# Kernel optimization log

Hardware: AMD Instinct MI355X
Metric: run time of the kernel (lower is better)

The kernel has to match this reference:

```python
import jax, jax.numpy as jnp
import numpy as np

B, N, C, H = 64, 197, 768, 12
CH = C // H            # 64 head dim
RC = CH // 2           # 32 reduced channel
RN = N // 8            # 24 reduced tokens
TOPK_COEF = 8
BUDGET = int(np.ceil(0.25 * N))   # 50
BASIS_THRESH = 0.02
MP_SCALE = H ** -0.5               # MaskPredictor: num_heads**-0.5 (as in source)
ATTN_SCALE = CH ** -0.5
LN_EPS = 1e-5


def _ln(x, g, b):
    mu = x.mean(-1, keepdims=True)
    var = ((x - mu) ** 2).mean(-1, keepdims=True)
    return (x - mu) * jax.lax.rsqrt(var + LN_EPS) * g + b


def _keep_topk(x, k):
    # zero all but the k largest along last axis (tie-break by value threshold)
    kth = jax.lax.top_k(x, k)[0][..., -1:]
    return jnp.where(x >= kth, x, 0.0)


def setup_inputs() -> dict:
    key = jax.random.key(0)
    ks = jax.random.split(key, 20)
    d = {}
    d['x'] = jax.random.normal(ks[0], (B, N, C), jnp.float32)
    s = 0.02
    d['Wqkv'] = jax.random.normal(ks[1], (C, 3 * C), jnp.float32) * s
    d['Wcq'] = jax.random.normal(ks[2], (CH, RC), jnp.float32) * s
    d['bcq'] = jnp.zeros((RC,), jnp.float32)
    d['Wck'] = jax.random.normal(ks[3], (CH, RC), jnp.float32) * s
    d['bck'] = jnp.zeros((RC,), jnp.float32)
    d['proj_n'] = jax.random.normal(ks[4], (N, RN), jnp.float32) * s
    d['proj_back_n'] = jax.random.normal(ks[5], (N, RN), jnp.float32) * s
    d['Wproj'] = jax.random.normal(ks[6], (C, C), jnp.float32) * s
    d['bproj'] = jnp.zeros((C,), jnp.float32)
    d['g1'] = jnp.ones((C,), jnp.float32)
    d['b1'] = jnp.zeros((C,), jnp.float32)
    d['g2'] = jnp.ones((C,), jnp.float32)
    d['b2'] = jnp.zeros((C,), jnp.float32)
    d['W1'] = jax.random.normal(ks[7], (C, 4 * C), jnp.float32) * s
    d['bfc1'] = jnp.zeros((4 * C,), jnp.float32)
    d['W2'] = jax.random.normal(ks[8], (4 * C, C), jnp.float32) * s
    d['bfc2'] = jnp.zeros((C,), jnp.float32)
    return d


def reference(x, Wqkv, Wcq, bcq, Wck, bck, proj_n, proj_back_n, Wproj, bproj,
              g1, b1, g2, b2, W1, bfc1, W2, bfc2):
    h = _ln(x, g1, b1)
    qkv = (h @ Wqkv).reshape(B, N, 3, H, CH).transpose(2, 0, 3, 1, 4)  # [3,B,H,N,CH]
    q, k, v = qkv[0], qkv[1], qkv[2]

    # ---- MaskPredictor (eval path) ----
    qp = q @ Wcq + bcq                                # [B,H,N,RC]
    kp = k @ Wck + bck                                # [B,H,N,RC]
    kk = jnp.einsum('bhnc,nr->bhcr', kp, proj_n)      # [B,H,RC,RN]
    cheap = jnp.einsum('bhnc,bhcr->bhnr', qp, kk) * MP_SCALE
    cheap = cheap[:, :, 1:, :]                        # drop cls query row
    basis_coef = jax.nn.softmax(cheap, axis=-1)       # [B,H,N-1,RN]
    basis_coef = _keep_topk(basis_coef, TOPK_COEF)
    basis = jnp.abs(proj_back_n.T)                    # [RN,N]
    basis = jnp.where(basis > BASIS_THRESH, basis, 0.0)
    approx_attn = basis_coef @ basis                  # [B,H,N-1,N]
    kth = jax.lax.top_k(approx_attn, BUDGET)[0][..., -1:]
    mask = approx_attn >= kth                         # [B,H,N-1,N] bool
    cls_mask = jnp.ones((B, H, 1, N), bool)
    attn_mask = jnp.concatenate([cls_mask, mask], axis=2)  # [B,H,N,N]

    # ---- masked full attention ----
    attn = jnp.einsum('bhqc,bhkc->bhqk', q * ATTN_SCALE, k)
    attn = jnp.where(attn_mask, attn, -jnp.inf)
    attn = jax.nn.softmax(attn, axis=-1)
    out = jnp.einsum('bhqk,bhkc->bhqc', attn, v)
    out = out.transpose(0, 2, 1, 3).reshape(B, N, C)
    out = out @ Wproj + bproj

    x = x + out                                       # skip_lam = 1.0
    h2 = _ln(x, g2, b2)
    mlp = jax.nn.gelu(h2 @ W1 + bfc1, approximate=False) @ W2 + bfc2
    x = x + mlp
    return x
```

## Files before the change

### kernel.cpp

```cpp
#include <hip/hip_runtime.h>
#include <math.h>
#include <float.h>

#define B_ 64
#define N_ 197
#define C_ 768
#define H_ 12
#define CH_ 64
#define RC_ 32
#define RN_ 24

typedef __attribute__((ext_vector_type(8))) short short8;
typedef __attribute__((ext_vector_type(4))) float f32x4;
typedef __attribute__((address_space(3))) void  lds_void;
typedef __attribute__((address_space(1))) const void g_void;

__device__ __forceinline__ float warp_sum(float v){
  #pragma unroll
  for(int o=32;o>=1;o>>=1) v += __shfl_xor(v,o);
  return v;
}
__device__ __forceinline__ float warp_max(float v){
  #pragma unroll
  for(int o=32;o>=1;o>>=1) v = fmaxf(v,__shfl_xor(v,o));
  return v;
}
__device__ __forceinline__ unsigned short f2bf(float f){
  union{float f; unsigned u;} c; c.f = f;
  unsigned r = c.u + 0x7FFF + ((c.u>>16)&1);
  return (unsigned short)(r>>16);
}
__device__ __forceinline__ float bf2f(unsigned short u){
  union{unsigned u; float f;} c; c.u = ((unsigned)u)<<16; return c.f;
}

__global__ __launch_bounds__(256) void ln_kernel(const float* __restrict__ x,
    const float* __restrict__ g, const float* __restrict__ bb, unsigned short* __restrict__ out){
  int r = blockIdx.x; int tid = threadIdx.x;
  const float* xr = x + (size_t)r*C_;
  float v0=xr[tid], v1=xr[tid+256], v2=xr[tid+512];
  __shared__ float red[8];
  float s = warp_sum(v0+v1+v2);
  if((tid&63)==0) red[tid>>6]=s;
  __syncthreads();
  float mu = (red[0]+red[1]+red[2]+red[3]) * (1.f/768.f);
  float d0=v0-mu,d1=v1-mu,d2=v2-mu;
  float s2 = warp_sum(d0*d0+d1*d1+d2*d2);
  if((tid&63)==0) red[4+(tid>>6)]=s2;
  __syncthreads();
  float rinv = rsqrtf((red[4]+red[5]+red[6]+red[7])*(1.f/768.f)+1e-5f);
  unsigned short* orow = out + (size_t)r*C_;
  orow[tid]     = f2bf(d0*rinv*g[tid]    +bb[tid]);
  orow[tid+256] = f2bf(d1*rinv*g[tid+256]+bb[tid+256]);
  orow[tid+512] = f2bf(d2*rinv*g[tid+512]+bb[tid+512]);
}

__global__ __launch_bounds__(256) void wtrans_kernel(const float* __restrict__ in,
    unsigned short* __restrict__ out, int K, int N){
  __shared__ float tile[32][33];
  int n0 = blockIdx.x*32, k0 = blockIdx.y*32;
  int tx = threadIdx.x&31, ty = threadIdx.x>>5;
  #pragma unroll
  for(int i=0;i<4;++i) tile[ty+8*i][tx] = in[(size_t)(k0+ty+8*i)*N + n0+tx];
  __syncthreads();
  #pragma unroll
  for(int i=0;i<4;++i) out[(size_t)(n0+ty+8*i)*K + k0+tx] = f2bf(tile[tx][ty+8*i]);
}

__global__ __launch_bounds__(256) void wcprep_kernel(const float* __restrict__ Wcq,
    const float* __restrict__ Wck, unsigned short* __restrict__ WcqT,
    unsigned short* __restrict__ WckT){
  int t = blockIdx.x*256 + threadIdx.x;
  if(t < 2048){
    int c = t>>6, k = t&63;
    WcqT[t] = f2bf(Wcq[k*32+c]);
    WckT[t] = f2bf(Wck[k*32+c]);
  }
}

template<int ACT, int RESID, int OUTBF16>
__global__ __launch_bounds__(256) void gemm_bf16(
    const unsigned short* __restrict__ A, const unsigned short* __restrict__ WT,
    const float* __restrict__ bias, const float* __restrict__ resid,
    void* __restrict__ Cout, int M, int K, int Nc){
  __shared__ unsigned short As[2*128*32];
  __shared__ unsigned short Bs[2*128*32];
  int tid = threadIdx.x, lane = tid&63, wid = tid>>6;
  int m0 = blockIdx.y*128, n0 = blockIdx.x*128;
  int wr = wid>>1, wc = wid&1;
  int lm = lane&15, lg = lane>>4;
  int row0 = tid>>2,         kc0 = (tid&3)*8;
  int row1 = (256+tid)>>2,   kc1 = (tid&3)*8;
  int ar0 = m0+row0; if(ar0 > M-1) ar0 = M-1;
  int ar1 = m0+row1; if(ar1 > M-1) ar1 = M-1;
  const unsigned short* gA0 = A  + (size_t)ar0*K + kc0;
  const unsigned short* gA1 = A  + (size_t)ar1*K + kc1;
  const unsigned short* gB0 = WT + (size_t)(n0+row0)*K + kc0;
  const unsigned short* gB1 = WT + (size_t)(n0+row1)*K + kc1;
  unsigned short* lA0 = As + (wid*64)*8;
  unsigned short* lA1 = As + (256 + wid*64)*8;
  unsigned short* lB0 = Bs + (wid*64)*8;
  unsigned short* lB1 = Bs + (256 + wid*64)*8;

#define STAGE_(buf, kt) do{ \
    __builtin_amdgcn_global_load_lds((g_void*)(gA0 + (kt)), (lds_void*)(lA0 + (buf)*4096), 16, 0, 0); \
    __builtin_amdgcn_global_load_lds((g_void*)(gB0 + (kt)), (lds_void*)(lB0 + (buf)*4096), 16, 0, 0); \
    __builtin_amdgcn_global_load_lds((g_void*)(gA1 + (kt)), (lds_void*)(lA1 + (buf)*4096), 16, 0, 0); \
    __builtin_amdgcn_global_load_lds((g_void*)(gB1 + (kt)), (lds_void*)(lB1 + (buf)*4096), 16, 0, 0); \
  }while(0)

  f32x4 acc[4][4] = {};
  const int nt = K/32;
  STAGE_(0, 0);
  __syncthreads();
  for(int t=0; t<nt; t+=2){
    STAGE_(1, (t+1)*32);
    {
      short8 af[4], bfv[4];
      #pragma unroll
      for(int i=0;i<4;++i){
        af[i]  = *(const short8*)(As + (64*wr + 16*i + lm)*32 + lg*8);
        bfv[i] = *(const short8*)(Bs + (64*wc + 16*i + lm)*32 + lg*8);
      }
      #pragma unroll
      for(int i=0;i<4;++i)
        #pragma unroll
        for(int j=0;j<4;++j)
          acc[i][j] = __builtin_amdgcn_mfma_f32_16x16x32_bf16(af[i], bfv[j], acc[i][j], 0,0,0);
    }
    __syncthreads();
    if(t+2 < nt) STAGE_(0, (t+2)*32);
    {
      short8 af[4], bfv[4];
      #pragma unroll
      for(int i=0;i<4;++i){
        af[i]  = *(const short8*)(As + 4096 + (64*wr + 16*i + lm)*32 + lg*8);
        bfv[i] = *(const short8*)(Bs + 4096 + (64*wc + 16*i + lm)*32 + lg*8);
      }
      #pragma unroll
      for(int i=0;i<4;++i)
        #pragma unroll
        for(int j=0;j<4;++j)
          acc[i][j] = __builtin_amdgcn_mfma_f32_16x16x32_bf16(af[i], bfv[j], acc[i][j], 0,0,0);
    }
    __syncthreads();
  }
#undef STAGE_
  #pragma unroll
  for(int i=0;i<4;++i){
    #pragma unroll
    for(int j=0;j<4;++j){
      int gcol = n0 + 64*wc + 16*j + lm;
      float bv = bias ? bias[gcol] : 0.f;
      #pragma unroll
      for(int r=0;r<4;++r){
        int grow = m0 + 64*wr + 16*i + lg*4 + r;
        if(grow < M){
          float cv = acc[i][j][r] + bv;
          if(ACT==1){
            float xx = cv;
            float p = xx*fmaf(xx*xx, 0.10294517f, 2.3022079f);
            float q = exp2f(p);
            cv = xx - xx*__builtin_amdgcn_rcpf(1.0f+q);
          }
          if(RESID) cv += resid[(size_t)grow*Nc + gcol];
          if(OUTBF16) ((unsigned short*)Cout)[(size_t)grow*Nc+gcol] = f2bf(cv);
          else        ((float*)Cout)[(size_t)grow*Nc+gcol] = cv;
        }
      }
    }
  }
}

__global__ __launch_bounds__(512) void cheap_kernel(
    const unsigned short* __restrict__ qkv,
    const unsigned short* __restrict__ WcqT, const float* __restrict__ bcq,
    const unsigned short* __restrict__ WckT, const float* __restrict__ bck,
    const float* __restrict__ proj_n, float* __restrict__ coef){
  int bh = blockIdx.x; int b = bh/H_, h = bh%H_;
  int tid = threadIdx.x, lane = tid&63, wv = tid>>6;
  int lm = lane&15, lg = lane>>4;
  __shared__ __align__(16) unsigned short KQ[208*64];
  __shared__ __align__(16) float P2T[32*212];
  __shared__ __align__(16) float PNT[24*200];
  __shared__ float KK[768];
  const unsigned short* Kbase = qkv + ((size_t)(b*N_)*3 + 1)*C_ + h*CH_;
  const unsigned short* Qbase = qkv + ((size_t)(b*N_)*3 + 0)*C_ + h*CH_;
  for(int idx = tid; idx < 208*32; idx += 512){
    int k = idx>>5, cp = idx&31;
    unsigned v = (k < N_) ? *(const unsigned*)(Kbase + (size_t)k*3*C_ + cp*2) : 0u;
    unsigned off = (unsigned)(k*128 + cp*4) ^ ((unsigned)(k&7)<<4);
    *(unsigned*)((char*)KQ + off) = v;
  }
  for(int idx = tid; idx < 24*200; idx += 512){
    int r = idx/200, n = idx - r*200;
    PNT[idx] = (n < N_) ? proj_n[n*24+r] : 0.f;
  }
  __syncthreads();
  {
    short8 bfr[2][2];
    #pragma unroll
    for(int j=0;j<2;++j)
      #pragma unroll
      for(int s=0;s<2;++s)
        bfr[j][s] = *(const short8*)(WckT + (j*16+lm)*64 + s*32 + lg*8);
    float bias[2] = { bck[lm], bck[16+lm] };
    for(int t=wv; t<13; t+=8){
      int row = t*16 + lm;
      unsigned o0 = (unsigned)(row*128 + lg*16) ^ ((unsigned)(row&7)<<4);
      unsigned o1 = (unsigned)(row*128 + 64 + lg*16) ^ ((unsigned)(row&7)<<4);
      short8 a0 = *(const short8*)((char*)KQ + o0);
      short8 a1 = *(const short8*)((char*)KQ + o1);
      #pragma unroll
      for(int j=0;j<2;++j){
        f32x4 acc = (f32x4){0.f,0.f,0.f,0.f};
        acc = __builtin_amdgcn_mfma_f32_16x16x32_bf16(a0, bfr[j][0], acc, 0,0,0);
        acc = __builtin_amdgcn_mfma_f32_16x16x32_bf16(a1, bfr[j][1], acc, 0,0,0);
        #pragma unroll
        for(int r=0;r<4;++r)
          P2T[(j*16+lm)*212 + t*16 + lg*4 + r] = acc[r] + bias[j];
      }
    }
  }
  __syncthreads();
  {
    int i0 = tid, i1 = tid + 512;
    bool has1 = (i1 < 768);
    int c0 = i0/24, r0 = i0 - c0*24;
    int c1 = has1 ? i1/24 : 0, r1 = has1 ? (i1 - (i1/24)*24) : 0;
    float a0=0.f, a1=0.f;
    for(int n=0;n<200;n+=4){
      float4 x0 = *(const float4*)&P2T[c0*212+n];
      float4 p0 = *(const float4*)&PNT[r0*200+n];
      a0 += x0.x*p0.x; a0 += x0.y*p0.y; a0 += x0.z*p0.z; a0 += x0.w*p0.w;
      if(has1){
        float4 x1 = *(const float4*)&P2T[c1*212+n];
        float4 p1 = *(const float4*)&PNT[r1*200+n];
        a1 += x1.x*p1.x; a1 += x1.y*p1.y; a1 += x1.z*p1.z; a1 += x1.w*p1.w;
      }
    }
    KK[i0] = a0;
    if(has1) KK[i1] = a1;
    for(int idx = tid; idx < 197*32; idx += 512){
      int k = idx>>5, cp = idx&31;
      unsigned v = *(const unsigned*)(Qbase + (size_t)k*3*C_ + cp*2);
      unsigned off = (unsigned)(k*128 + cp*4) ^ ((unsigned)(k&7)<<4);
      *(unsigned*)((char*)KQ + off) = v;
    }
  }
  __syncthreads();
  float* QP = P2T;
  {
    short8 bfr[2][2];
    #pragma unroll
    for(int j=0;j<2;++j)
      #pragma unroll
      for(int s=0;s<2;++s)
        bfr[j][s] = *(const short8*)(WcqT + (j*16+lm)*64 + s*32 + lg*8);
    float bias[2] = { bcq[lm], bcq[16+lm] };
    for(int t=wv; t<13; t+=8){
      int row = t*16 + lm;
      unsigned o0 = (unsigned)(row*128 + lg*16) ^ ((unsigned)(row&7)<<4);
      unsigned o1 = (unsigned)(row*128 + 64 + lg*16) ^ ((unsigned)(row&7)<<4);
      short8 a0 = *(const short8*)((char*)KQ + o0);
      short8 a1 = *(const short8*)((char*)KQ + o1);
      #pragma unroll
      for(int j=0;j<2;++j){
        f32x4 acc = (f32x4){0.f,0.f,0.f,0.f};
        acc = __builtin_amdgcn_mfma_f32_16x16x32_bf16(a0, bfr[j][0], acc, 0,0,0);
        acc = __builtin_amdgcn_mfma_f32_16x16x32_bf16(a1, bfr[j][1], acc, 0,0,0);
        #pragma unroll
        for(int r=0;r<4;++r)
          QP[(t*16 + lg*4 + r)*32 + j*16 + lm] = acc[r] + bias[j];
      }
    }
  }
  __syncthreads();
  int l32 = lane & 31, half = lane >> 5;
  bool act = l32 < RN_;
  int ll = act ? l32 : 0;
  float kkreg[32];
  #pragma unroll
  for(int c=0;c<32;++c) kkreg[c] = KK[c*24 + ll];
  for(int i2 = wv*2; i2 < 196; i2 += 16){
    int i = i2 + half;
    int n = i + 1;
    float accv = 0.f;
    #pragma unroll
    for(int q=0;q<8;++q){
      float4 v4 = *(const float4*)&QP[n*32 + q*4];
      accv += v4.x*kkreg[q*4];   accv += v4.y*kkreg[q*4+1];
      accv += v4.z*kkreg[q*4+2]; accv += v4.w*kkreg[q*4+3];
    }
    float val = act ? accv * 0.28867513459481287f : -INFINITY;
    float m = val;
    #pragma unroll
    for(int o=16;o>=1;o>>=1) m = fmaxf(m, __shfl_xor(m, o));
    float e = act ? expf(val - m) : 0.f;
    float ssum = e;
    #pragma unroll
    for(int o=16;o>=1;o>>=1) ssum += __shfl_xor(ssum, o);
    float p = e/ssum;
    unsigned u = __float_as_uint(e);
    unsigned pL=0, pH=0;
    #pragma unroll
    for(int bit=30; bit>=0; --bit){
      unsigned tL = pL | (1u<<bit), tH = pH | (1u<<bit);
      unsigned thr = half ? tH : tL;
      unsigned long long bal = __ballot(u >= thr);
      int cL = __popcll(bal & 0xFFFFFFull);
      int cH = __popcll((bal>>32) & 0xFFFFFFull);
      if(cL>=8) pL=tL;
      if(cH>=8) pH=tH;
    }
    unsigned myp = half ? pH : pL;
    if(act) coef[((size_t)bh*196 + i)*24 + l32] = (u >= myp) ? p : 0.f;
  }
}

__global__ __launch_bounds__(256) void basis_kernel(const float* __restrict__ pb,
    float* __restrict__ basis){
  int t = blockIdx.x*256 + threadIdx.x;
  if(t < RN_*N_){
    int r = t/N_, j = t%N_;
    float v = fabsf(pb[(size_t)j*RN_ + r]);
    basis[t] = (v > 0.02f) ? v : 0.f;
  }
}

__global__ __launch_bounds__(256) void mask4_kernel(const float* __restrict__ coef,
    const float* __restrict__ basis, unsigned int* __restrict__ maskw){
  __shared__ float Bs[24*256];
  int tid = threadIdx.x, lane = tid&63, wv = tid>>6;
  for(int idx = tid; idx < 24*256; idx += 256){
    int r = idx>>8, q = idx&255;
    int e = ((q&3)<<6) | (q>>2);
    Bs[idx] = (e < N_) ? basis[r*N_ + e] : 0.f;
  }
  __syncthreads();
  int rowbase = blockIdx.x*16 + wv*4;
  #pragma unroll
  for(int j=0;j<4;++j){
    int row = rowbase + j;
    int qi = row % N_; int bh = row / N_;
    if(qi==0){
      if(lane<8){
        unsigned v = (lane<6)?0xFFFFFFFFu:((lane==6)?0x1Fu:0u);
        maskw[(size_t)row*8+lane]=v;
      }
      continue;
    }
    float cfv = (lane<24) ? coef[((size_t)bh*196 + (qi-1))*24 + lane] : 0.f;
    unsigned long long nz = __ballot(cfv != 0.f);
    float4 av = make_float4(0.f,0.f,0.f,0.f);
    while(nz){
      int r = __ffsll((unsigned long long)nz) - 1;
      nz &= nz - 1;
      float c = __uint_as_float(__builtin_amdgcn_readlane(__float_as_uint(cfv), r));
      float4 bv = *(const float4*)&Bs[r*256 + lane*4];
      av.x += c*bv.x; av.y += c*bv.y; av.z += c*bv.z; av.w += c*bv.w;
    }
    unsigned u0=__float_as_uint(av.x), u1=__float_as_uint(av.y);
    unsigned u2=__float_as_uint(av.z), u3=__float_as_uint(av.w);
    unsigned prefix = 0;
    #pragma unroll
    for(int bit=30; bit>=0; --bit){
      unsigned t = prefix | (1u<<bit);
      int c = __popcll(__ballot(u0 >= t)) + __popcll(__ballot(u1 >= t))
            + __popcll(__ballot(u2 >= t)) + __popcll(__ballot(u3 >= t));
      if(c >= 50) prefix = t;
    }
    unsigned uu[4] = {u0,u1,u2,u3};
    #pragma unroll
    for(int r=0;r<4;++r){
      bool valid = (r<3) | (lane<5);
      bool keep = valid && (uu[r] >= prefix);
      unsigned long long bal = __ballot(keep);
      if(lane==0){
        maskw[(size_t)row*8 + 2*r]   = (unsigned)(bal & 0xFFFFFFFFull);
        maskw[(size_t)row*8 + 2*r+1] = (unsigned)(bal>>32);
      }
    }
  }
}

__global__ __launch_bounds__(512) void attn3_kernel(const unsigned short* __restrict__ qkv,
    const unsigned int* __restrict__ maskw, unsigned short* __restrict__ attn_out){
  int bh = blockIdx.x; int b = bh/H_, h = bh%H_;
  int tid = threadIdx.x, lane = tid&63, wv = tid>>6;
  int g = lane>>4, c16 = lane&15;
  __shared__ unsigned short Kb[208*64];
  __shared__ unsigned short Vt[64*220];
  __shared__ unsigned short Pl[8*16*224];
  __shared__ unsigned int   Ml[8][16][8];
  const unsigned short* Kbase = qkv + ((size_t)(b*N_)*3 + 1)*C_ + h*CH_;
  const unsigned short* Vbase = qkv + ((size_t)(b*N_)*3 + 2)*C_ + h*CH_;
  for(int idx = tid; idx < 208*32; idx += 512){
    int k = idx>>5, cp = idx&31;
    unsigned pk = 0;
    if(k < N_) pk = *(const unsigned*)(Kbase + (size_t)k*3*C_ + cp*2);
    unsigned off = (unsigned)(k*128 + cp*4) ^ ((unsigned)(k&7)<<4);
    *(unsigned*)((char*)Kb + off) = pk;
  }
  for(int idx = tid; idx < 64*110; idx += 512){
    int kp = idx>>6, c = idx&63;
    int k0 = kp*2, k1 = kp*2+1;
    unsigned v0 = (k0<N_) ? Vbase[(size_t)k0*3*C_ + c] : 0;
    unsigned v1 = (k1<N_) ? Vbase[(size_t)k1*3*C_ + c] : 0;
    *(unsigned*)((char*)Vt + c*440 + kp*4) = v0 | (v1<<16);
  }
  __syncthreads();
  size_t pbase = (size_t)wv*16*448;
  for(int i=lane;i<128;i+=64){
    int ql = i>>3; int kk = 208 + (i&7)*2;
    unsigned off = (unsigned)(ql*448 + kk*2) ^ ((unsigned)(ql&7)<<4);
    *(unsigned*)((char*)Pl + pbase + off) = 0u;
  }
  for(int t = wv; t < 13; t += 8){
    int qb = t*16;
    for(int i = lane; i < 128; i += 64){
      int row = i>>3, word = i&7;
      int qr = qb+row; if(qr>196) qr=196;
      Ml[wv][row][word] = maskw[(size_t)(bh*N_+qr)*8 + word];
    }
    int qrow = qb + c16; if(qrow>196) qrow=196;
    const unsigned short* Qr = qkv + ((size_t)(b*N_+qrow)*3)*C_ + h*CH_ + g*8;
    short8 af[2];
    af[0] = *(const short8*)(Qr);
    af[1] = *(const short8*)(Qr + 32);
    f32x4 sf[13];
    #pragma unroll
    for(int f=0;f<13;++f){
      sf[f] = (f32x4){0.f,0.f,0.f,0.f};
      #pragma unroll
      for(int s=0;s<2;++s){
        int row = f*16 + c16;
        unsigned off = (unsigned)(row*128 + s*64 + g*16) ^ ((unsigned)(row&7)<<4);
        short8 bfr = *(const short8*)((char*)Kb + off);
        sf[f] = __builtin_amdgcn_mfma_f32_16x16x32_bf16(af[s], bfr, sf[f], 0,0,0);
      }
      sf[f][0]*=0.125f; sf[f][1]*=0.125f; sf[f][2]*=0.125f; sf[f][3]*=0.125f;
    }
    unsigned keep[4] = {0,0,0,0};
    float m[4] = {-FLT_MAX,-FLT_MAX,-FLT_MAX,-FLT_MAX};
    #pragma unroll
    for(int f=0;f<13;++f)
      #pragma unroll
      for(int r=0;r<4;++r){
        unsigned bit = (Ml[wv][g*4+r][f>>1] >> ((f&1)*16 + c16)) & 1u;
        keep[r] |= bit<<f;
        if(bit) m[r] = fmaxf(m[r], sf[f][r]);
      }
    #pragma unroll
    for(int r=0;r<4;++r){
      #pragma unroll
      for(int o=8;o>=1;o>>=1) m[r] = fmaxf(m[r], __shfl_xor(m[r], o));
    }
    float sum[4] = {0,0,0,0};
    #pragma unroll
    for(int f=0;f<13;++f)
      #pragma unroll
      for(int r=0;r<4;++r){
        float e = ((keep[r]>>f)&1u) ? expf(sf[f][r]-m[r]) : 0.f;
        sf[f][r] = e; sum[r] += e;
      }
    #pragma unroll
    for(int r=0;r<4;++r){
      #pragma unroll
      for(int o=8;o>=1;o>>=1) sum[r] += __shfl_xor(sum[r], o);
      sum[r] = 1.f/sum[r];
    }
    #pragma unroll
    for(int f=0;f<13;++f)
      #pragma unroll
      for(int r=0;r<4;++r){
        int ql = g*4+r;
        unsigned off = (unsigned)(ql*448 + (f*16+c16)*2) ^ ((unsigned)(ql&7)<<4);
        *(unsigned short*)((char*)Pl + pbase + off) = f2bf(sf[f][r]*sum[r]);
      }
    #pragma unroll
    for(int ct=0;ct<4;++ct){
      f32x4 oa = (f32x4){0.f,0.f,0.f,0.f};
      #pragma unroll
      for(int ks=0;ks<7;++ks){
        unsigned offa = (unsigned)(c16*448 + (ks*32+g*8)*2) ^ ((unsigned)(c16&7)<<4);
        short8 pa = *(const short8*)((char*)Pl + pbase + offa);
        short8 vb = *(const short8*)((char*)Vt + (size_t)(ct*16+c16)*440 + (ks*32+g*8)*2);
        oa = __builtin_amdgcn_mfma_f32_16x16x32_bf16(pa, vb, oa, 0,0,0);
      }
      #pragma unroll
      for(int r=0;r<4;++r){
        int qq = qb + g*4 + r;
        if(qq < N_)
          attn_out[((size_t)(b*N_+qq))*C_ + h*CH_ + ct*16 + c16] = f2bf(oa[r]);
      }
    }
  }
}

extern "C" void kernel_launch(void* const* d_in, const int* in_sizes, int n_in,
                              void* d_out, int out_size, void* d_ws, size_t ws_size,
                              hipStream_t stream){
  const float* x    =(const float*)d_in[0];
  const float* Wqkv =(const float*)d_in[1];
  const float* Wcq  =(const float*)d_in[2];
  const float* bcq  =(const float*)d_in[3];
  const float* Wck  =(const float*)d_in[4];
  const float* bck  =(const float*)d_in[5];
  const float* proj_n=(const float*)d_in[6];
  const float* proj_back_n=(const float*)d_in[7];
  const float* Wproj=(const float*)d_in[8];
  const float* bproj=(const float*)d_in[9];
  const float* g1=(const float*)d_in[10];
  const float* b1=(const float*)d_in[11];
  const float* g2=(const float*)d_in[12];
  const float* b2=(const float*)d_in[13];
  const float* W1=(const float*)d_in[14];
  const float* bfc1=(const float*)d_in[15];
  const float* W2=(const float*)d_in[16];
  const float* bfc2=(const float*)d_in[17];
  float* out=(float*)d_out;

  float* ws=(float*)d_ws;
  size_t off=0;
  unsigned short* hbuf = (unsigned short*)(ws+off); off += (size_t)12608*768/2;
  size_t qkv_off = off;
  unsigned short* qkv = (unsigned short*)(ws+off); off += (size_t)12608*2304/2;
  off += (size_t)768*197*32;
  off += (size_t)768*197*32;
  off += (size_t)768*32*24;
  float* coef = ws+off;        off += (size_t)768*196*24;
  float* basis= ws+off;        off += 4736;
  unsigned int* maskw=(unsigned int*)(ws+off); off += (size_t)768*197*8;
  unsigned short* WqkvT = (unsigned short*)(ws+off); off += (size_t)2304*768/2;
  unsigned short* WprojT= (unsigned short*)(ws+off); off += (size_t)768*768/2;
  unsigned short* W1T   = (unsigned short*)(ws+off); off += (size_t)3072*768/2;
  unsigned short* W2T   = (unsigned short*)(ws+off); off += (size_t)768*3072/2;
  unsigned short* WcqT  = (unsigned short*)(ws+off); off += 1024;
  unsigned short* WckT  = (unsigned short*)(ws+off); off += 1024;
  unsigned short* attn_out = hbuf;
  unsigned short* hidden = (unsigned short*)(ws+qkv_off);
  float* x1 = out;

  wtrans_kernel<<<dim3(72,24),256,0,stream>>>(Wqkv, WqkvT, 768, 2304);
  wtrans_kernel<<<dim3(24,24),256,0,stream>>>(Wproj, WprojT, 768, 768);
  wtrans_kernel<<<dim3(96,24),256,0,stream>>>(W1, W1T, 768, 3072);
  wtrans_kernel<<<dim3(24,96),256,0,stream>>>(W2, W2T, 3072, 768);
  wcprep_kernel<<<8,256,0,stream>>>(Wcq, Wck, WcqT, WckT);
  ln_kernel<<<12608,256,0,stream>>>(x,g1,b1,hbuf);
  gemm_bf16<0,0,1><<<dim3(18,99),256,0,stream>>>(hbuf,WqkvT,nullptr,nullptr,qkv,12608,768,2304);
  cheap_kernel<<<768,512,0,stream>>>(qkv,WcqT,bcq,WckT,bck,proj_n,coef);
  basis_kernel<<<19,256,0,stream>>>(proj_back_n,basis);
  mask4_kernel<<<9456,256,0,stream>>>(coef,basis,maskw);
  attn3_kernel<<<768,512,0,stream>>>(qkv,maskw,attn_out);
  gemm_bf16<0,1,0><<<dim3(6,99),256,0,stream>>>(attn_out,WprojT,bproj,x,x1,12608,768,768);
  ln_kernel<<<12608,256,0,stream>>>(x1,g2,b2,hbuf);
  gemm_bf16<1,0,1><<<dim3(24,99),256,0,stream>>>(hbuf,W1T,bfc1,nullptr,hidden,12608,768,3072);
  gemm_bf16<0,1,0><<<dim3(6,99),256,0,stream>>>(hidden,W2T,bfc2,x1,out,12608,3072,768);
}
```

Baseline: 725.4 us.

## Retile bf16 GEMM to 256x256x64 tiles with 8 waves and swizzled LDS

```diff
diff --git a/kernel.cpp b/kernel.cpp
--- a/kernel.cpp
+++ b/kernel.cpp
@@ -79,82 +79,80 @@
 }
 
 template<int ACT, int RESID, int OUTBF16>
-__global__ __launch_bounds__(256) void gemm_bf16(
+__global__ __launch_bounds__(512, 2) void gemm_bf16(
     const unsigned short* __restrict__ A, const unsigned short* __restrict__ WT,
     const float* __restrict__ bias, const float* __restrict__ resid,
     void* __restrict__ Cout, int M, int K, int Nc){
-  __shared__ unsigned short As[2*128*32];
-  __shared__ unsigned short Bs[2*128*32];
+  __shared__ unsigned short As[2*256*64];
+  __shared__ unsigned short Bs[2*256*64];
   int tid = threadIdx.x, lane = tid&63, wid = tid>>6;
-  int m0 = blockIdx.y*128, n0 = blockIdx.x*128;
-  int wr = wid>>1, wc = wid&1;
+  int m0 = blockIdx.y*256, n0 = blockIdx.x*256;
+  int wm = wid>>2, wn = wid&3;
   int lm = lane&15, lg = lane>>4;
-  int row0 = tid>>2,         kc0 = (tid&3)*8;
-  int row1 = (256+tid)>>2,   kc1 = (tid&3)*8;
-  int ar0 = m0+row0; if(ar0 > M-1) ar0 = M-1;
-  int ar1 = m0+row1; if(ar1 > M-1) ar1 = M-1;
-  const unsigned short* gA0 = A  + (size_t)ar0*K + kc0;
-  const unsigned short* gA1 = A  + (size_t)ar1*K + kc1;
-  const unsigned short* gB0 = WT + (size_t)(n0+row0)*K + kc0;
-  const unsigned short* gB1 = WT + (size_t)(n0+row1)*K + kc1;
-  unsigned short* lA0 = As + (wid*64)*8;
-  unsigned short* lA1 = As + (256 + wid*64)*8;
-  unsigned short* lB0 = Bs + (wid*64)*8;
-  unsigned short* lB1 = Bs + (256 + wid*64)*8;
-
-#define STAGE_(buf, kt) do{ \
-    __builtin_amdgcn_global_load_lds((g_void*)(gA0 + (kt)), (lds_void*)(lA0 + (buf)*4096), 16, 0, 0); \
-    __builtin_amdgcn_global_load_lds((g_void*)(gB0 + (kt)), (lds_void*)(lB0 + (buf)*4096), 16, 0, 0); \
-    __builtin_amdgcn_global_load_lds((g_void*)(gA1 + (kt)), (lds_void*)(lA1 + (buf)*4096), 16, 0, 0); \
-    __builtin_amdgcn_global_load_lds((g_void*)(gB1 + (kt)), (lds_void*)(lB1 + (buf)*4096), 16, 0, 0); \
+  int srow = tid>>3;
+  int schk = (tid&7) ^ (srow&7);
+  const unsigned short* ga[4]; const unsigned short* gb[4];
+  #pragma unroll
+  for(int ld=0; ld<4; ++ld){
+    int ar = m0 + ld*64 + srow; if(ar > M-1) ar = M-1;
+    ga[ld] = A  + (size_t)ar*K + schk*8;
+    gb[ld] = WT + (size_t)(n0 + ld*64 + srow)*K + schk*8;
+  }
+  unsigned short* lA = As + wid*512;
+  unsigned short* lB = Bs + wid*512;
+
+#define STAGE8(buf, kt) do{ \
+    _Pragma("unroll") \
+    for(int ld=0; ld<4; ++ld){ \
+      __builtin_amdgcn_global_load_lds((g_void*)(ga[ld] + (kt)), (lds_void*)(lA + (buf)*16384 + ld*4096), 16, 0, 0); \
+      __builtin_amdgcn_global_load_lds((g_void*)(gb[ld] + (kt)), (lds_void*)(lB + (buf)*16384 + ld*4096), 16, 0, 0); \
+    } \
   }while(0)
 
-  f32x4 acc[4][4] = {};
-  const int nt = K/32;
-  STAGE_(0, 0);
-  __syncthreads();
-  for(int t=0; t<nt; t+=2){
-    STAGE_(1, (t+1)*32);
-    {
-      short8 af[4], bfv[4];
-      #pragma unroll
-      for(int i=0;i<4;++i){
-        af[i]  = *(const short8*)(As + (64*wr + 16*i + lm)*32 + lg*8);
-        bfv[i] = *(const short8*)(Bs + (64*wc + 16*i + lm)*32 + lg*8);
-      }
-      #pragma unroll
-      for(int i=0;i<4;++i)
+  f32x4 acc[8][4] = {};
+  const int nt = K/64;
+  STAGE8(0, 0);
+  __syncthreads();
+  for(int t=0; t<nt; ++t){
+    int buf = t&1;
+    if(t+1 < nt) STAGE8(buf^1, (t+1)*64);
+    const char* abase = (const char*)As + buf*32768;
+    const char* bbase = (const char*)Bs + buf*32768;
+    #pragma unroll
+    for(int s=0; s<2; ++s){
+      int chunk = ((s*4+lg) ^ (lm&7)) * 16;
+      short8 af[8];
+      #pragma unroll
+      for(int i=0;i<8;++i){
+        int rA = wm*128 + i*16 + lm;
+        af[i] = *(const short8*)(abase + rA*128 + chunk);
+      }
+      #pragma unroll
+      for(int np=0; np<2; ++np){
+        int rB0 = wn*64 + np*32 + lm;
+        short8 bf0 = *(const short8*)(bbase + rB0*128 + chunk);
+        short8 bf1 = *(const short8*)(bbase + (rB0+16)*128 + chunk);
+        __builtin_amdgcn_s_setprio(1);
         #pragma unroll
-        for(int j=0;j<4;++j)
-          acc[i][j] = __builtin_amdgcn_mfma_f32_16x16x32_bf16(af[i], bfv[j], acc[i][j], 0,0,0);
+        for(int i=0;i<8;++i){
+          acc[i][np*2]   = __builtin_amdgcn_mfma_f32_16x16x32_bf16(af[i], bf0, acc[i][np*2],   0,0,0);
+          acc[i][np*2+1] = __builtin_amdgcn_mfma_f32_16x16x32_bf16(af[i], bf1, acc[i][np*2+1], 0,0,0);
+        }
+        __builtin_amdgcn_s_setprio(0);
+      }
     }
     __syncthreads();
-    if(t+2 < nt) STAGE_(0, (t+2)*32);
-    {
-      short8 af[4], bfv[4];
-      #pragma unroll
-      for(int i=0;i<4;++i){
-        af[i]  = *(const short8*)(As + 4096 + (64*wr + 16*i + lm)*32 + lg*8);
-        bfv[i] = *(const short8*)(Bs + 4096 + (64*wc + 16*i + lm)*32 + lg*8);
-      }
-      #pragma unroll
-      for(int i=0;i<4;++i)
-        #pragma unroll
-        for(int j=0;j<4;++j)
-          acc[i][j] = __builtin_amdgcn_mfma_f32_16x16x32_bf16(af[i], bfv[j], acc[i][j], 0,0,0);
-    }
-    __syncthreads();
-  }
-#undef STAGE_
-  #pragma unroll
-  for(int i=0;i<4;++i){
+  }
+#undef STAGE8
+  #pragma unroll
+  for(int i=0;i<8;++i){
     #pragma unroll
     for(int j=0;j<4;++j){
-      int gcol = n0 + 64*wc + 16*j + lm;
+      int gcol = n0 + wn*64 + j*16 + lm;
       float bv = bias ? bias[gcol] : 0.f;
       #pragma unroll
       for(int r=0;r<4;++r){
-        int grow = m0 + 64*wr + 16*i + lg*4 + r;
+        int grow = m0 + wm*128 + i*16 + lg*4 + r;
         if(grow < M){
           float cv = acc[i][j][r] + bv;
           if(ACT==1){
@@ -548,13 +546,13 @@
   wtrans_kernel<<<dim3(24,96),256,0,stream>>>(W2, W2T, 3072, 768);
   wcprep_kernel<<<8,256,0,stream>>>(Wcq, Wck, WcqT, WckT);
   ln_kernel<<<12608,256,0,stream>>>(x,g1,b1,hbuf);
-  gemm_bf16<0,0,1><<<dim3(18,99),256,0,stream>>>(hbuf,WqkvT,nullptr,nullptr,qkv,12608,768,2304);
+  gemm_bf16<0,0,1><<<dim3(9,50),512,0,stream>>>(hbuf,WqkvT,nullptr,nullptr,qkv,12608,768,2304);
   cheap_kernel<<<768,512,0,stream>>>(qkv,WcqT,bcq,WckT,bck,proj_n,coef);
   basis_kernel<<<19,256,0,stream>>>(proj_back_n,basis);
   mask4_kernel<<<9456,256,0,stream>>>(coef,basis,maskw);
   attn3_kernel<<<768,512,0,stream>>>(qkv,maskw,attn_out);
-  gemm_bf16<0,1,0><<<dim3(6,99),256,0,stream>>>(attn_out,WprojT,bproj,x,x1,12608,768,768);
+  gemm_bf16<0,1,0><<<dim3(3,50),512,0,stream>>>(attn_out,WprojT,bproj,x,x1,12608,768,768);
   ln_kernel<<<12608,256,0,stream>>>(x1,g2,b2,hbuf);
-  gemm_bf16<1,0,1><<<dim3(24,99),256,0,stream>>>(hbuf,W1T,bfc1,nullptr,hidden,12608,768,3072);
-  gemm_bf16<0,1,0><<<dim3(6,99),256,0,stream>>>(hidden,W2T,bfc2,x1,out,12608,3072,768);
-}
+  gemm_bf16<1,0,1><<<dim3(12,50),512,0,stream>>>(hbuf,W1T,bfc1,nullptr,hidden,12608,768,3072);
+  gemm_bf16<0,1,0><<<dim3(3,50),512,0,stream>>>(hidden,W2T,bfc2,x1,out,12608,3072,768);
+}
```

Result: slower. 781.2 us (+7.7%).

## Add 256x256-tile bf16 GEMM for QKV and FC1 projections

Applied to the files above, without the earlier changes.

```diff
diff --git a/kernel.cpp b/kernel.cpp
--- a/kernel.cpp
+++ b/kernel.cpp
@@ -172,6 +172,89 @@
   }
 }
 
+template<int ACT, int RESID, int OUTBF16>
+__global__ __launch_bounds__(512, 4) void gemm256_bf16(
+    const unsigned short* __restrict__ A, const unsigned short* __restrict__ WT,
+    const float* __restrict__ bias, const float* __restrict__ resid,
+    void* __restrict__ Cout, int M, int K, int Nc){
+  __shared__ unsigned short As[2*256*32];
+  __shared__ unsigned short Bs[2*256*32];
+  int tid = threadIdx.x, lane = tid&63, wid = tid>>6;
+  int m0 = blockIdx.y*256, n0 = blockIdx.x*256;
+  int wm = wid>>2, wn = wid&3;
+  int lm = lane&15, lg = lane>>4;
+  int row0 = tid>>2,       kc0 = (tid&3)*8;
+  int row1 = (512+tid)>>2, kc1 = (tid&3)*8;
+  int arA0 = m0+row0; if(arA0 > M-1) arA0 = M-1;
+  int arA1 = m0+row1; if(arA1 > M-1) arA1 = M-1;
+  const unsigned short* gA0 = A  + (size_t)arA0*K + kc0;
+  const unsigned short* gA1 = A  + (size_t)arA1*K + kc1;
+  const unsigned short* gB0 = WT + (size_t)(n0+row0)*K + kc0;
+  const unsigned short* gB1 = WT + (size_t)(n0+row1)*K + kc1;
+  unsigned short* lA0 = As + wid*512;
+  unsigned short* lA1 = As + 4096 + wid*512;
+  unsigned short* lB0 = Bs + wid*512;
+  unsigned short* lB1 = Bs + 4096 + wid*512;
+
+#define STAGE2_(buf, kt) do{ \
+    __builtin_amdgcn_global_load_lds((g_void*)(gA0 + (kt)), (lds_void*)(lA0 + (buf)*8192), 16, 0, 0); \
+    __builtin_amdgcn_global_load_lds((g_void*)(gB0 + (kt)), (lds_void*)(lB0 + (buf)*8192), 16, 0, 0); \
+    __builtin_amdgcn_global_load_lds((g_void*)(gA1 + (kt)), (lds_void*)(lA1 + (buf)*8192), 16, 0, 0); \
+    __builtin_amdgcn_global_load_lds((g_void*)(gB1 + (kt)), (lds_void*)(lB1 + (buf)*8192), 16, 0, 0); \
+  }while(0)
+
+  f32x4 acc[8][4] = {};
+  const int nt = K/32;
+  STAGE2_(0, 0);
+  __syncthreads();
+  for(int t=0; t<nt; ++t){
+    int buf = t&1;
+    if(t+1 < nt) STAGE2_(buf^1, (t+1)*32);
+    const unsigned short* abase = As + buf*8192;
+    const unsigned short* bbase = Bs + buf*8192;
+    short8 af[8], bfv[4];
+    #pragma unroll
+    for(int i=0;i<8;++i)
+      af[i] = *(const short8*)(abase + (wm*128 + i*16 + lm)*32 + lg*8);
+    #pragma unroll
+    for(int j=0;j<4;++j)
+      bfv[j] = *(const short8*)(bbase + (wn*64 + j*16 + lm)*32 + lg*8);
+    __builtin_amdgcn_s_setprio(1);
+    #pragma unroll
+    for(int i=0;i<8;++i)
+      #pragma unroll
+      for(int j=0;j<4;++j)
+        acc[i][j] = __builtin_amdgcn_mfma_f32_16x16x32_bf16(af[i], bfv[j], acc[i][j], 0,0,0);
+    __builtin_amdgcn_s_setprio(0);
+    __syncthreads();
+  }
+#undef STAGE2_
+  #pragma unroll
+  for(int i=0;i<8;++i){
+    #pragma unroll
+    for(int j=0;j<4;++j){
+      int gcol = n0 + wn*64 + j*16 + lm;
+      float bv = bias ? bias[gcol] : 0.f;
+      #pragma unroll
+      for(int r=0;r<4;++r){
+        int grow = m0 + wm*128 + i*16 + lg*4 + r;
+        if(grow < M){
+          float cv = acc[i][j][r] + bv;
+          if(ACT==1){
+            float xx = cv;
+            float p = xx*fmaf(xx*xx, 0.10294517f, 2.3022079f);
+            float q = exp2f(p);
+            cv = xx - xx*__builtin_amdgcn_rcpf(1.0f+q);
+          }
+          if(RESID) cv += resid[(size_t)grow*Nc + gcol];
+          if(OUTBF16) ((unsigned short*)Cout)[(size_t)grow*Nc+gcol] = f2bf(cv);
+          else        ((float*)Cout)[(size_t)grow*Nc+gcol] = cv;
+        }
+      }
+    }
+  }
+}
+
 __global__ __launch_bounds__(512) void cheap_kernel(
     const unsigned short* __restrict__ qkv,
     const unsigned short* __restrict__ WcqT, const float* __restrict__ bcq,
@@ -548,13 +631,13 @@
   wtrans_kernel<<<dim3(24,96),256,0,stream>>>(W2, W2T, 3072, 768);
   wcprep_kernel<<<8,256,0,stream>>>(Wcq, Wck, WcqT, WckT);
   ln_kernel<<<12608,256,0,stream>>>(x,g1,b1,hbuf);
-  gemm_bf16<0,0,1><<<dim3(18,99),256,0,stream>>>(hbuf,WqkvT,nullptr,nullptr,qkv,12608,768,2304);
+  gemm256_bf16<0,0,1><<<dim3(9,50),512,0,stream>>>(hbuf,WqkvT,nullptr,nullptr,qkv,12608,768,2304);
   cheap_kernel<<<768,512,0,stream>>>(qkv,WcqT,bcq,WckT,bck,proj_n,coef);
   basis_kernel<<<19,256,0,stream>>>(proj_back_n,basis);
   mask4_kernel<<<9456,256,0,stream>>>(coef,basis,maskw);
   attn3_kernel<<<768,512,0,stream>>>(qkv,maskw,attn_out);
   gemm_bf16<0,1,0><<<dim3(6,99),256,0,stream>>>(attn_out,WprojT,bproj,x,x1,12608,768,768);
   ln_kernel<<<12608,256,0,stream>>>(x1,g2,b2,hbuf);
-  gemm_bf16<1,0,1><<<dim3(24,99),256,0,stream>>>(hbuf,W1T,bfc1,nullptr,hidden,12608,768,3072);
+  gemm256_bf16<1,0,1><<<dim3(12,50),512,0,stream>>>(hbuf,W1T,bfc1,nullptr,hidden,12608,768,3072);
   gemm_bf16<0,1,0><<<dim3(6,99),256,0,stream>>>(hidden,W2T,bfc2,x1,out,12608,3072,768);
 }
```

After: 1.762 ms. 2.43x slower.
